# Kernel optimization log

Hardware: AMD Instinct MI355X
Metric: run time of the kernel (lower is better)

The kernel has to match this reference:

```python
import jax, jax.numpy as jnp
import numpy as np

B, K, N = 8192, 10, 100
LAM = 1.0


def _vec_transpose_P():
    # 9x9 vec-transpose permutation: P[3i+j, 3j+i] = 1 (the _getP matrix)
    P = np.zeros((9, 9), dtype=np.float32)
    for i in range(3):
        for j in range(3):
            P[3 * i + j, 3 * j + i] = 1.0
    return jnp.asarray(P)


def setup_inputs() -> dict:
    key = jax.random.key(0)
    k1, k2, k3 = jax.random.split(key, 3)
    weights = jax.random.uniform(k1, (N, 1), dtype=jnp.float32) + 0.1  # positive weights
    model_keypoints = jax.random.normal(k2, (K, 3, N), dtype=jnp.float32)
    y = jax.random.normal(k3, (B, 3, N), dtype=jnp.float32)
    return {"y": y, "weights": weights, "model_keypoints": model_keypoints}


def _pace_forward(y, weights, model_keypoints):
    n = model_keypoints.shape[-1]
    k = model_keypoints.shape[0]
    bsz = y.shape[0]
    w = weights                                  # (N,1)
    wsum = w.sum()
    b = model_keypoints                          # (K,3,N)
    b_w = (b @ w) / wsum                         # (K,3,1)
    sw = jnp.sqrt(w[:, 0])                       # (N,)

    # ---- precomputed constants (original __init__) ----
    bar_b = sw[None, None, :] * (b - b_w)                    # (K,3,N)
    bar_B = bar_b.transpose(0, 2, 1).reshape(k, 3 * n).T     # (3N,K), row idx 3n+a
    bar_H = 2.0 * (bar_B.T @ bar_B + LAM * jnp.eye(k, dtype=y.dtype))
    Hinv = jnp.linalg.inv(bar_H)
    Ht = Hinv @ jnp.ones((k, 1), dtype=y.dtype)
    denom = Ht.sum()
    G = Hinv - (Ht @ Ht.T) / denom               # (K,K)
    g = Ht / denom                               # (K,1)
    GBt = G @ bar_B.T                            # (K,3N)
    M = jnp.concatenate([2.0 * bar_B @ GBt - jnp.eye(3 * n, dtype=y.dtype),
                         2.0 * jnp.sqrt(LAM) * GBt], axis=0)       # (3N+K,3N)
    h = jnp.concatenate([bar_B @ g, jnp.sqrt(LAM) * g], axis=0)    # (3N+K,1)
    P = _vec_transpose_P().astype(y.dtype)

    # ---- forward ----
    y_w = (y @ w) / wsum                         # (B,3,1)
    bar_y = sw[None, None, :] * (y - y_w)        # (B,3,N)

    # E_b = M @ kron(Ybar_b^T, I3) @ P, done batched without materializing kron:
    # (M @ kron(Y^T, I3))[m, 3j+a] = sum_n M[m, 3n+a] * Y[j, n]
    Mr = M.reshape(-1, n, 3)                                  # Mr[m, nn, a] = M[m, 3nn+a]
    MB = jnp.einsum('mna,bjn->bmja', Mr, bar_y)               # (B,3N+K,3,3)
    E = MB.reshape(bsz, -1, 9) @ P                            # (B,3N+K,9)
    q00 = h[:, 0] @ h[:, 0]                                   # scalar h^T h
    hE = jnp.einsum('m,bmc->bc', h[:, 0], E)                  # (B,9)
    Q11 = jnp.einsum('bmc,bmd->bcd', E, E)                    # (B,9,9)
    top = jnp.concatenate([jnp.broadcast_to(q00, (bsz, 1, 1)), hE[:, None, :]], axis=2)
    bot = jnp.concatenate([hE[:, :, None], Q11], axis=2)
    Q = jnp.concatenate([top, bot], axis=1)                   # (B,10,10)

    # SDP relaxation: at a tight optimum X = v v^T with v the minimizer of v^T Q v,
    # recovered here as the eigenvector of Q with smallest eigenvalue (batched eigh)
    _, evec = jnp.linalg.eigh(Q)
    v = evec[:, :, 0]                                         # (B,10), ascending order
    v = v / v[:, :1]                                          # homogenize: v[0] = 1
    R = v[:, 1:].reshape(bsz, 3, 3).transpose(0, 2, 1)        # (B,3,3)

    # shape coefficients: c = 2 * G B^T * kron(I_N, R^T) vec(bar_y) + g
    RTy = jnp.einsum('bra,brn->bna', R, bar_y).reshape(bsz, 3 * n)   # idx 3n+a
    c = 2.0 * jnp.einsum('km,bm->bk', GBt, RTy)[:, :, None] + g[None, :, :]  # (B,K,1)
    # translation: t = y_w - R b_w^T c
    t = y_w - R @ jnp.einsum('ka,bko->bao', b_w[:, :, 0], c)  # (B,3,1)
    return R, t, c


def reference(y, weights, model_keypoints):
    return _pace_forward(y, weights, model_keypoints)
```

## Files before the change

### kernel.cpp

```cpp
#include <hip/hip_runtime.h>
#include <math.h>

#define SM_WSUM 0
#define SM_RWS  1
#define SM_Q00  2
#define SM_Z2   4
#define SM_BS   16
#define SM_W    48
#define SM_G    148
#define SM_GV   248
#define SM_BW   260
#define SM_SIZE 292

__host__ __device__ constexpr int TRI(int p,int q){ return p*10-(p*(p+1))/2+q; }
__host__ __device__ constexpr int SIDX(int a,int b){ return (a<=b)?TRI(a,b):TRI(b,a); }
__host__ __device__ constexpr int LTRI(int i,int j){ return i*(i+1)/2+j; }

template<int CTRL>
__device__ __forceinline__ float dpp_add(float v){
  int s = __builtin_amdgcn_mov_dpp(__float_as_int(v), CTRL, 0xF, 0xF, true);
  return v + __int_as_float(s);
}
__device__ __forceinline__ float gsum8(float v){
  v = dpp_add<0xB1>(v);
  v = dpp_add<0x4E>(v);
  v = dpp_add<0x141>(v);
  return v;
}

__global__ __launch_bounds__(64,1) void pace_fused(const float* __restrict__ y,
                                                   const float* __restrict__ w,
                                                   const float* __restrict__ mk,
                                                   float* __restrict__ out){
  __shared__ __attribute__((aligned(16))) float sc[3600];
  __shared__ float sm[SM_SIZE];
  __shared__ __attribute__((aligned(16))) float scr[3712];
  const int tid  = threadIdx.x;
  const int sub  = tid & 7;
  const int item = tid >> 3;
  const int gb   = blockIdx.x*8 + item;
  const float* yb = y + gb*300;

  {
    float* s_mb = scr;
    float* s_w  = scr+3000;
    float* s_sw = scr+3104;
    float* s_bw = scr+3208;
    float* s_C  = scr+3240;
    float* s_Hi = scr+3340;
    float* s_G  = scr+3440;
    float* s_T  = scr+3540;
    float* s_gv = scr+3640;
    float* s_Ht = scr+3656;
    float* s_z  = scr+3672;

    for (int i=tid;i<3000;i+=64) s_mb[i]=mk[i];
    for (int i=tid;i<100;i+=64){ float x=w[i]; s_w[i]=x; s_sw[i]=sqrtf(x); }
    __syncthreads();

    float a = s_w[tid] + ((tid<36)? s_w[tid+64] : 0.f);
    #pragma unroll
    for (int m=32;m;m>>=1) a += __shfl_xor(a,m);
    const float wsum = a;
    const float rws = 1.0f/a;

    if (tid<30){
      const float4* p=(const float4*)&s_mb[tid*100];
      const float4* q=(const float4*)&s_w[0];
      float acc=0;
      #pragma unroll 5
      for (int j=0;j<25;j++){ float4 x=p[j], yv=q[j];
        acc=fmaf(x.x,yv.x,acc); acc=fmaf(x.y,yv.y,acc);
        acc=fmaf(x.z,yv.z,acc); acc=fmaf(x.w,yv.w,acc); }
      s_bw[tid]=acc*rws;
    }
    __syncthreads();
    for (int i=tid;i<3000;i+=64){ int r=i/100, n=i-r*100; s_mb[i]=s_sw[n]*(s_mb[i]-s_bw[r]); }
    __syncthreads();
    for (int e=tid;e<100;e+=64){
      int k=e/10, k2=e-10*k;
      const float4* p1=(const float4*)&s_mb[k*300];
      const float4* p2=(const float4*)&s_mb[k2*300];
      float acc=0;
      #pragma unroll 5
      for (int j=0;j<75;j++){ float4 x=p1[j], yv=p2[j];
        acc=fmaf(x.x,yv.x,acc); acc=fmaf(x.y,yv.y,acc);
        acc=fmaf(x.z,yv.z,acc); acc=fmaf(x.w,yv.w,acc); }
      s_C[e]=acc;
    }
    __syncthreads();
    float R[20];
    {
      int row=(tid<10)? tid : 0;
      #pragma unroll
      for (int c=0;c<10;c++) R[c]=2.0f*(s_C[row*10+c]+(c==row?1.0f:0.0f));
      #pragma unroll
      for (int c=0;c<10;c++) R[10+c]=(c==row)?1.0f:0.0f;
    }
    #pragma unroll
    for (int p=0;p<10;p++){
      float appv=__shfl(R[p],p);
      float ra=1.0f/appv;
      float fr=R[p];
      #pragma unroll
      for (int c=0;c<20;c++){
        float pc=__shfl(R[c],p)*ra;
        R[c]=(tid==p)? pc : fmaf(-fr,pc,R[c]);
      }
    }
    float ht=0.f;
    if (tid<10){
      #pragma unroll
      for (int c=0;c<10;c++){ s_Hi[tid*10+c]=R[10+c]; ht+=R[10+c]; }
      s_Ht[tid]=ht;
    }
    float hv=(tid<10)? ht : 0.f;
    #pragma unroll
    for (int m=32;m;m>>=1) hv+=__shfl_xor(hv,m);
    const float rden=1.0f/hv;
    if (tid<10) s_gv[tid]=ht*rden;
    __syncthreads();
    for (int e=tid;e<100;e+=64){ int r=e/10,c=e-10*r; s_G[e]=s_Hi[e]-s_Ht[r]*s_Ht[c]*rden; }
    __syncthreads();
    for (int e=tid;e<100;e+=64){
      int r=e/10,c=e-10*r; float acc=0;
      #pragma unroll
      for (int j=0;j<10;j++) acc+=(s_C[r*10+j]+(r==j?1.0f:0.0f))*s_G[j*10+c];
      s_T[e]=acc;
    }
    __syncthreads();
    for (int e=tid;e<100;e+=64){
      int r=e/10,c=e-10*r; float acc=0;
      #pragma unroll
      for (int j=0;j<10;j++) acc+=s_G[r*10+j]*s_T[j*10+c];
      sm[SM_W+e]=4.0f*acc-4.0f*s_G[e];
      sm[SM_G+e]=s_G[e];
    }
    if (tid<10){
      float acc=0;
      #pragma unroll
      for (int j=0;j<10;j++) acc+=(s_C[tid*10+j]+(tid==j?1.0f:0.0f))*s_gv[j];
      s_z[tid]=acc;
    }
    __syncthreads();
    if (tid<10){
      float acc=0;
      #pragma unroll
      for (int j=0;j<10;j++) acc+=s_G[tid*10+j]*s_z[j];
      sm[SM_Z2+tid]=2.0f*acc-s_gv[tid];
    }
    float qv=0.f;
    if (tid<10){
      float acc=0;
      #pragma unroll
      for (int c=0;c<10;c++) acc+=s_C[tid*10+c]*s_gv[c];
      qv=s_gv[tid]*acc+s_gv[tid]*s_gv[tid];
    }
    #pragma unroll
    for (int m=32;m;m>>=1) qv+=__shfl_xor(qv,m);
    if (tid==0){ sm[SM_WSUM]=wsum; sm[SM_RWS]=rws; sm[SM_Q00]=qv; sm[3]=0.f; }
    for (int i=tid;i<3600;i+=64){
      int n=i/36, e=i-36*n; float v;
      if (e==0) v=s_w[n];
      else if (e>=31) v=0.f;
      else v=s_mb[(e-1)*100+n]*s_sw[n];
      sc[i]=v;
    }
    if (tid<30){
      const float4* p=(const float4*)&s_mb[tid*100];
      const float4* q=(const float4*)&s_sw[0];
      float acc=0;
      #pragma unroll 5
      for (int j=0;j<25;j++){ float4 x=p[j], yv=q[j];
        acc=fmaf(x.x,yv.x,acc); acc=fmaf(x.y,yv.y,acc);
        acc=fmaf(x.z,yv.z,acc); acc=fmaf(x.w,yv.w,acc); }
      sm[SM_BS+tid]=acc;
    }
    if (tid<10) sm[SM_GV+tid]=s_gv[tid];
    if (tid<30) sm[SM_BW+tid]=s_bw[tid];
    __syncthreads();
  }

  float* sF  = scr;
  float* sD  = scr+736;
  float* sQl = scr+832;
  float* sG3 = scr+1280;

  float F0[90];
  #pragma unroll
  for (int i=0;i<90;i++) F0[i]=0.f;
  float swy0=0,swy1=0,swy2=0,s00=0,s01=0,s02=0,s11=0,s12=0,s22=0;

  #pragma unroll
  for (int mrep=0;mrep<4;++mrep){
    int g=sub+8*mrep;
    if (g<25){
      float4 a4=*(const float4*)(yb+4*g);
      float4 b4=*(const float4*)(yb+100+4*g);
      float4 g4=*(const float4*)(yb+200+4*g);
      float ax[4]={a4.x,a4.y,a4.z,a4.w};
      float bx[4]={b4.x,b4.y,b4.z,b4.w};
      float gx[4]={g4.x,g4.y,g4.z,g4.w};
      #pragma unroll
      for (int u=0;u<4;u++){
        const float* cf=&sc[(4*g+u)*36];
        float c[32];
        #pragma unroll
        for (int r=0;r<8;r++) ((float4*)c)[r]=((const float4*)cf)[r];
        float y0=ax[u],y1=bx[u],y2=gx[u];
        float wn=c[0];
        float wy0=wn*y0,wy1=wn*y1,wy2=wn*y2;
        swy0+=wy0;swy1+=wy1;swy2+=wy2;
        s00+=wy0*y0;s01+=wy0*y1;s02+=wy0*y2;s11+=wy1*y1;s12+=wy1*y2;s22+=wy2*y2;
        #pragma unroll
        for (int k=0;k<10;k++){
          #pragma unroll
          for (int j=0;j<3;j++){
            float bcv=c[1+k*3+j];
            F0[k*9+j*3+0]+=bcv*y0;
            F0[k*9+j*3+1]+=bcv*y1;
            F0[k*9+j*3+2]+=bcv*y2;
          }
        }
      }
    }
  }
  #pragma unroll
  for (int e=0;e<90;e++) F0[e]=gsum8(F0[e]);
  swy0=gsum8(swy0); swy1=gsum8(swy1); swy2=gsum8(swy2);
  s00=gsum8(s00); s01=gsum8(s01); s02=gsum8(s02);
  s11=gsum8(s11); s12=gsum8(s12); s22=gsum8(s22);

  const float wsum=sm[SM_WSUM], rws=sm[SM_RWS];
  const float yw0=swy0*rws, yw1=swy1*rws, yw2=swy2*rws;
  float G3r[9];
  G3r[0]=s00-wsum*yw0*yw0; G3r[4]=s11-wsum*yw1*yw1; G3r[8]=s22-wsum*yw2*yw2;
  G3r[1]=G3r[3]=s01-wsum*yw0*yw1;
  G3r[2]=G3r[6]=s02-wsum*yw0*yw2;
  G3r[5]=G3r[7]=s12-wsum*yw1*yw2;
  #pragma unroll
  for (int k=0;k<10;k++){
    float bs0=sm[SM_BS+k*3+0],bs1=sm[SM_BS+k*3+1],bs2=sm[SM_BS+k*3+2];
    F0[k*9+0]-=yw0*bs0; F0[k*9+1]-=yw1*bs0; F0[k*9+2]-=yw2*bs0;
    F0[k*9+3]-=yw0*bs1; F0[k*9+4]-=yw1*bs1; F0[k*9+5]-=yw2*bs1;
    F0[k*9+6]-=yw0*bs2; F0[k*9+7]-=yw1*bs2; F0[k*9+8]-=yw2*bs2;
  }
  if (sub==0){
    #pragma unroll
    for (int e=0;e<90;e++) sF[item*90+e]=F0[e];
    #pragma unroll
    for (int e=0;e<9;e++) sG3[item*9+e]=G3r[e];
  }
  __syncthreads();

  {
    int mp=sub;
    float fcol[10], t2[10];
    #pragma unroll
    for (int k=0;k<10;k++) fcol[k]=sF[item*90+k*9+mp];
    #pragma unroll
    for (int k=0;k<10;k++){
      float acc=0;
      #pragma unroll
      for (int k2=0;k2<10;k2++) acc+=sm[SM_W+k*10+k2]*fcol[k2];
      t2[k]=acc;
    }
    float he=0;
    #pragma unroll
    for (int k=0;k<10;k++) he+=sm[SM_Z2+k]*fcol[k];
    sQl[item*56 + 1+mp]=he;
    #pragma unroll 1
    for (int m=0;m<=mp;m++){
      float gd=sG3[item*9+(m%3)*3+(mp%3)];
      float acc=((m/3)==(mp/3))? gd : 0.f;
      #pragma unroll
      for (int k=0;k<10;k++) acc+=sF[item*90+k*9+m]*t2[k];
      int p=1+m, q=1+mp;
      sQl[item*56 + p*10-((p*(p+1))>>1)+q]=acc;
    }
    if (sub==0){
      mp=8;
      #pragma unroll
      for (int k=0;k<10;k++) fcol[k]=sF[item*90+k*9+mp];
      #pragma unroll
      for (int k=0;k<10;k++){
        float acc=0;
        #pragma unroll
        for (int k2=0;k2<10;k2++) acc+=sm[SM_W+k*10+k2]*fcol[k2];
        t2[k]=acc;
      }
      he=0;
      #pragma unroll
      for (int k=0;k<10;k++) he+=sm[SM_Z2+k]*fcol[k];
      sQl[item*56 + 9]=he;
      #pragma unroll 1
      for (int m=0;m<=8;m++){
        float gd=sG3[item*9+(m%3)*3+2];
        float acc=((m/3)==2)? gd : 0.f;
        #pragma unroll
        for (int k=0;k<10;k++) acc+=sF[item*90+k*9+m]*t2[k];
        int p=1+m, q=9;
        sQl[item*56 + p*10-((p*(p+1))>>1)+q]=acc;
      }
      sQl[item*56 + 0]=sm[SM_Q00];
    }
  }
  __syncthreads();

  float A[55];
  #pragma unroll
  for (int e=0;e<55;e++) A[e]=sQl[item*56+e];
  float dd[10], ee[9];
  #pragma unroll
  for (int k=0;k<8;k++){
    float nrm2=0.f;
    #pragma unroll
    for (int i=1;i<10;i++){ if (i<k+1) continue; float xi=A[SIDX(i,k)]; nrm2=fmaf(xi,xi,nrm2); }
    float x0=A[SIDX(k+1,k)];
    float nr=sqrtf(nrm2);
    float alpha=-copysignf(nr,x0);
    bool ok=nrm2>1e-30f;
    float v1=x0-alpha;
    float vtv=-2.0f*alpha*v1;
    float bh=ok?2.0f*__builtin_amdgcn_rcpf(vtv):0.f;
    ee[k]=ok?alpha:x0;
    float vv[10];
    #pragma unroll
    for (int i=0;i<10;i++) vv[i]=(i<k+1)?0.f:((i==k+1)?v1:A[SIDX(i,k)]);
    float p[10];
    #pragma unroll
    for (int i=0;i<10;i++){
      if (i<k+1){ p[i]=0.f; continue; }
      float acc=0;
      #pragma unroll
      for (int j=1;j<10;j++){ if (j<k+1) continue; acc+=A[SIDX(i,j)]*vv[j]; }
      p[i]=bh*acc;
    }
    float Kc=0.f;
    #pragma unroll
    for (int i=1;i<10;i++){ if (i<k+1) continue; Kc=fmaf(vv[i],p[i],Kc); }
    Kc*=0.5f*bh;
    float wv[10];
    #pragma unroll
    for (int i=0;i<10;i++) wv[i]=p[i]-Kc*vv[i];
    #pragma unroll
    for (int i=1;i<10;i++){
      if (i<k+1) continue;
      #pragma unroll
      for (int j=1;j<10;j++){
        if (j<i) continue;
        A[TRI(i,j)]-=vv[i]*wv[j]+wv[i]*vv[j];
      }
    }
  }
  ee[8]=A[TRI(8,9)];
  #pragma unroll
  for (int i=0;i<10;i++) dd[i]=A[TRI(i,i)];
  float esq[9];
  #pragma unroll
  for (int i=0;i<9;i++) esq[i]=ee[i]*ee[i];

  float scaleT=0.f, lo=1e30f, hi=1e30f;
  #pragma unroll
  for (int i=0;i<10;i++){
    float r=((i>0)?fabsf(ee[i-1]):0.f)+((i<9)?fabsf(ee[i]):0.f);
    scaleT=fmaxf(scaleT,fabsf(dd[i])+r);
    lo=fminf(lo,dd[i]-r);
    hi=fminf(hi,dd[i]);
  }
  hi+=1e-6f*scaleT+1e-30f;
  const float pm=1e-12f*scaleT+1e-37f;
  const float r9=1.0f/9.0f;
  #pragma unroll 1
  for (int it=0;it<6;++it){
    float delta=(hi-lo)*r9;
    float mid=lo+delta*(float)(sub+1);
    float q=dd[0]-mid;
    q=(fabsf(q)<pm)?((q<0.f)?-pm:pm):q;
    int cnt=(q<0.f);
    #pragma unroll
    for (int i=1;i<10;i++){
      q=dd[i]-mid-esq[i-1]*__builtin_amdgcn_rcpf(q);
      q=(fabsf(q)<pm)?((q<0.f)?-pm:pm):q;
      cnt+=(q<0.f);
    }
    unsigned long long bal=__ballot(cnt>0);
    unsigned gb8=(unsigned)((bal>>(item*8))&0xFFull);
    int js=gb8?(__ffs((int)gb8)-1):8;
    float nhi=(js<8)?(lo+delta*(float)(js+1)):hi;
    lo=lo+delta*(float)js;
    hi=nhi;
  }
  const float sigma=lo-1e-5f*scaleT-1e-30f;
  const float pmL=1e-8f*scaleT+1e-37f;

  float Lc[55], rd[10];
  #pragma unroll
  for (int i=0;i<10;i++){
    #pragma unroll
    for (int j=0;j<10;j++){
      if (j>i) continue;
      float a=sQl[item*56+SIDX(j,i)]-((i==j)?sigma:0.f);
      #pragma unroll
      for (int t2=0;t2<9;t2++){
        if (t2>=j) continue;
        a-=Lc[LTRI(i,t2)]*Lc[LTRI(j,t2)];
      }
      if (j<i) Lc[LTRI(i,j)]=a*rd[j];
      else { a=fmaxf(a,pmL); rd[i]=rsqrtf(a); Lc[LTRI(i,i)]=a*rd[i]; }
    }
  }
  float xv[10];
  #pragma unroll
  for (int i=0;i<10;i++) xv[i]=1.f;
  #pragma unroll 1
  for (int itr=0;itr<3;++itr){
    #pragma unroll
    for (int i=0;i<10;i++){
      float acc=xv[i];
      #pragma unroll
      for (int j=0;j<9;j++){ if (j>=i) continue; acc-=Lc[LTRI(i,j)]*xv[j]; }
      acc*=rd[i];
      xv[i]=fminf(fmaxf(acc,-1e15f),1e15f);
    }
    #pragma unroll
    for (int i=9;i>=0;i--){
      float acc=xv[i];
      #pragma unroll
      for (int j=9;j>0;j--){ if (j<=i) continue; acc-=Lc[LTRI(j,i)]*xv[j]; }
      acc*=rd[i];
      xv[i]=fminf(fmaxf(acc,-1e15f),1e15f);
    }
    float nn=0.f;
    #pragma unroll
    for (int i=0;i<10;i++) nn=fmaf(xv[i],xv[i],nn);
    nn=fmaxf(nn,1e-30f);
    float sc2=rsqrtf(nn);
    #pragma unroll
    for (int i=0;i<10;i++) xv[i]*=sc2;
  }
  float r0=1.0f/xv[0];
  float vn[10];
  vn[0]=1.f;
  #pragma unroll
  for (int m=1;m<10;m++) vn[m]=xv[m]*r0;

  {
    float dv=0;
    #pragma unroll
    for (int m=0;m<9;m++) dv+=vn[1+m]*sF[item*90+sub*9+m];
    sD[item*10+sub]=dv;
    if (sub<2){
      float dv2=0;
      #pragma unroll
      for (int m=0;m<9;m++) dv2+=vn[1+m]*sF[item*90+(8+sub)*9+m];
      sD[item*10+8+sub]=dv2;
    }
  }
  __syncthreads();
  float dreg[10];
  #pragma unroll
  for (int k=0;k<10;k++) dreg[k]=sD[item*10+k];
  __syncthreads();
  {
    float acc=0;
    #pragma unroll
    for (int k2=0;k2<10;k2++) acc+=sm[SM_G+sub*10+k2]*dreg[k2];
    float cvk=2.0f*acc+sm[SM_GV+sub];
    out[98304+gb*10+sub]=cvk;
    sD[item*10+sub]=cvk;
    if (sub<2){
      int kk=8+sub;
      float acc2=0;
      #pragma unroll
      for (int k2=0;k2<10;k2++) acc2+=sm[SM_G+kk*10+k2]*dreg[k2];
      float cvk2=2.0f*acc2+sm[SM_GV+kk];
      out[98304+gb*10+kk]=cvk2;
      sD[item*10+kk]=cvk2;
    }
  }
  __syncthreads();
  float cvr[10];
  #pragma unroll
  for (int k=0;k<10;k++) cvr[k]=sD[item*10+k];
  float e0=0,e1=0,e2=0;
  #pragma unroll
  for (int k=0;k<10;k++){
    e0+=sm[SM_BW+k*3+0]*cvr[k];
    e1+=sm[SM_BW+k*3+1]*cvr[k];
    e2+=sm[SM_BW+k*3+2]*cvr[k];
  }
  if (sub==2){
    #pragma unroll
    for (int i=0;i<3;i++)
      #pragma unroll
      for (int j=0;j<3;j++)
        out[gb*9+i*3+j]=vn[1+3*j+i];
  }
  if (sub==3){
    out[73728+gb*3+0]=yw0-(vn[1]*e0+vn[4]*e1+vn[7]*e2);
    out[73728+gb*3+1]=yw1-(vn[2]*e0+vn[5]*e1+vn[8]*e2);
    out[73728+gb*3+2]=yw2-(vn[3]*e0+vn[6]*e1+vn[9]*e2);
  }
}

extern "C" void kernel_launch(void* const* d_in, const int* in_sizes, int n_in,
                              void* d_out, int out_size, void* d_ws, size_t ws_size,
                              hipStream_t stream) {
  const float* y  = (const float*)d_in[0];
  const float* w  = (const float*)d_in[1];
  const float* mk = (const float*)d_in[2];
  float* out = (float*)d_out;
  pace_fused<<<1024, 64, 0, stream>>>(y, w, mk, out);
}
```

Baseline: 104.6 us.

## Use 16 lanes per batch item, shrink shared scratch, double grid

Each batch item now gets 16 lanes instead of 8, so a 64-thread block handles 4 items and the grid doubles to 2048 blocks. The per-point accumulation, reductions (gsum16), Q-row construction, bisection (17 intervals, 5 iterations) and final outputs are remapped to the wider group. The preamble no longer stages the full model-keypoint array in LDS: it computes C directly from global memory and writes the weighted coefficients straight into sc, which shrinks shared scratch to allow 2 blocks per CU. The trade-off is that every block now repeats the per-block constant preprocessing, twice as many blocks run it, and more global reads are made in the preamble.

```diff
diff --git a/kernel.cpp b/kernel.cpp
--- a/kernel.cpp
+++ b/kernel.cpp
@@ -12,6 +12,21 @@
 #define SM_BW   260
 #define SM_SIZE 292
 
+#define AR_W    0
+#define AR_BW   104
+#define AR_C    136
+#define AR_HI   240
+#define AR_G    340
+#define AR_T    440
+#define AR_GV   544
+#define AR_HT   560
+#define AR_Z    576
+#define AR_F    0
+#define AR_QL   360
+#define AR_D    592
+#define AR_G3   640
+#define AR_SIZE 768
+
 __host__ __device__ constexpr int TRI(int p,int q){ return p*10-(p*(p+1))/2+q; }
 __host__ __device__ constexpr int SIDX(int a,int b){ return (a<=b)?TRI(a,b):TRI(b,a); }
 __host__ __device__ constexpr int LTRI(int i,int j){ return i*(i+1)/2+j; }
@@ -21,79 +36,95 @@
   int s = __builtin_amdgcn_mov_dpp(__float_as_int(v), CTRL, 0xF, 0xF, true);
   return v + __int_as_float(s);
 }
-__device__ __forceinline__ float gsum8(float v){
+__device__ __forceinline__ float gsum16(float v){
   v = dpp_add<0xB1>(v);
   v = dpp_add<0x4E>(v);
   v = dpp_add<0x141>(v);
+  v = dpp_add<0x140>(v);
   return v;
 }
 
-__global__ __launch_bounds__(64,1) void pace_fused(const float* __restrict__ y,
+__global__ __launch_bounds__(64,2) void pace_fused(const float* __restrict__ y,
                                                    const float* __restrict__ w,
                                                    const float* __restrict__ mk,
                                                    float* __restrict__ out){
   __shared__ __attribute__((aligned(16))) float sc[3600];
   __shared__ float sm[SM_SIZE];
-  __shared__ __attribute__((aligned(16))) float scr[3712];
+  __shared__ __attribute__((aligned(16))) float arena[AR_SIZE];
   const int tid  = threadIdx.x;
-  const int sub  = tid & 7;
-  const int item = tid >> 3;
-  const int gb   = blockIdx.x*8 + item;
+  const int sub  = tid & 15;
+  const int item = tid >> 4;
+  const int gb   = blockIdx.x*4 + item;
   const float* yb = y + gb*300;
 
   {
-    float* s_mb = scr;
-    float* s_w  = scr+3000;
-    float* s_sw = scr+3104;
-    float* s_bw = scr+3208;
-    float* s_C  = scr+3240;
-    float* s_Hi = scr+3340;
-    float* s_G  = scr+3440;
-    float* s_T  = scr+3540;
-    float* s_gv = scr+3640;
-    float* s_Ht = scr+3656;
-    float* s_z  = scr+3672;
-
-    for (int i=tid;i<3000;i+=64) s_mb[i]=mk[i];
-    for (int i=tid;i<100;i+=64){ float x=w[i]; s_w[i]=x; s_sw[i]=sqrtf(x); }
-    __syncthreads();
-
-    float a = s_w[tid] + ((tid<36)? s_w[tid+64] : 0.f);
-    #pragma unroll
-    for (int m=32;m;m>>=1) a += __shfl_xor(a,m);
-    const float wsum = a;
-    const float rws = 1.0f/a;
+    float* a_w  = arena+AR_W;
+    float* a_bw = arena+AR_BW;
+    float* a_C  = arena+AR_C;
+    float* a_Hi = arena+AR_HI;
+    float* a_G  = arena+AR_G;
+    float* a_T  = arena+AR_T;
+    float* a_gv = arena+AR_GV;
+    float* a_Ht = arena+AR_HT;
+    float* a_z  = arena+AR_Z;
+
+    for (int i=tid;i<100;i+=64) a_w[i]=w[i];
+    __syncthreads();
+
+    float av = a_w[tid] + ((tid<36)? a_w[tid+64] : 0.f);
+    #pragma unroll
+    for (int m=32;m;m>>=1) av += __shfl_xor(av,m);
+    const float wsum = av;
+    const float rws  = 1.0f/av;
 
     if (tid<30){
-      const float4* p=(const float4*)&s_mb[tid*100];
-      const float4* q=(const float4*)&s_w[0];
+      const float4* p=(const float4*)(mk+tid*100);
+      const float4* q=(const float4*)a_w;
       float acc=0;
       #pragma unroll 5
       for (int j=0;j<25;j++){ float4 x=p[j], yv=q[j];
         acc=fmaf(x.x,yv.x,acc); acc=fmaf(x.y,yv.y,acc);
         acc=fmaf(x.z,yv.z,acc); acc=fmaf(x.w,yv.w,acc); }
-      s_bw[tid]=acc*rws;
-    }
-    __syncthreads();
-    for (int i=tid;i<3000;i+=64){ int r=i/100, n=i-r*100; s_mb[i]=s_sw[n]*(s_mb[i]-s_bw[r]); }
-    __syncthreads();
+      a_bw[tid]=acc*rws;
+    }
+    __syncthreads();
+
+    for (int i=tid;i<3000;i+=64){
+      int r=i/100, n=i-100*r;
+      sc[n*36+1+r]=a_w[n]*(mk[i]-a_bw[r]);
+    }
+    for (int i=tid;i<100;i+=64){
+      sc[i*36]=a_w[i];
+      sc[i*36+31]=0.f; sc[i*36+32]=0.f; sc[i*36+33]=0.f;
+      sc[i*36+34]=0.f; sc[i*36+35]=0.f;
+    }
     for (int e=tid;e<100;e+=64){
       int k=e/10, k2=e-10*k;
-      const float4* p1=(const float4*)&s_mb[k*300];
-      const float4* p2=(const float4*)&s_mb[k2*300];
-      float acc=0;
-      #pragma unroll 5
-      for (int j=0;j<75;j++){ float4 x=p1[j], yv=p2[j];
-        acc=fmaf(x.x,yv.x,acc); acc=fmaf(x.y,yv.y,acc);
-        acc=fmaf(x.z,yv.z,acc); acc=fmaf(x.w,yv.w,acc); }
-      s_C[e]=acc;
-    }
-    __syncthreads();
+      float acc=0;
+      #pragma unroll
+      for (int j=0;j<3;j++){
+        const float4* pa=(const float4*)(mk+(3*k+j)*100);
+        const float4* pb=(const float4*)(mk+(3*k2+j)*100);
+        const float4* pw=(const float4*)a_w;
+        float ba=a_bw[3*k+j], bb=a_bw[3*k2+j];
+        #pragma unroll 5
+        for (int q=0;q<25;q++){
+          float4 xa=pa[q], xb=pb[q], xw=pw[q];
+          acc=fmaf(xw.x*(xa.x-ba),(xb.x-bb),acc);
+          acc=fmaf(xw.y*(xa.y-ba),(xb.y-bb),acc);
+          acc=fmaf(xw.z*(xa.z-ba),(xb.z-bb),acc);
+          acc=fmaf(xw.w*(xa.w-ba),(xb.w-bb),acc);
+        }
+      }
+      a_C[e]=acc;
+    }
+    __syncthreads();
+
     float R[20];
     {
       int row=(tid<10)? tid : 0;
       #pragma unroll
-      for (int c=0;c<10;c++) R[c]=2.0f*(s_C[row*10+c]+(c==row?1.0f:0.0f));
+      for (int c=0;c<10;c++) R[c]=2.0f*(a_C[row*10+c]+(c==row?1.0f:0.0f));
       #pragma unroll
       for (int c=0;c<10;c++) R[10+c]=(c==row)?1.0f:0.0f;
     }
@@ -111,125 +142,104 @@
     float ht=0.f;
     if (tid<10){
       #pragma unroll
-      for (int c=0;c<10;c++){ s_Hi[tid*10+c]=R[10+c]; ht+=R[10+c]; }
-      s_Ht[tid]=ht;
+      for (int c=0;c<10;c++){ a_Hi[tid*10+c]=R[10+c]; ht+=R[10+c]; }
+      a_Ht[tid]=ht;
     }
     float hv=(tid<10)? ht : 0.f;
     #pragma unroll
     for (int m=32;m;m>>=1) hv+=__shfl_xor(hv,m);
     const float rden=1.0f/hv;
-    if (tid<10) s_gv[tid]=ht*rden;
-    __syncthreads();
-    for (int e=tid;e<100;e+=64){ int r=e/10,c=e-10*r; s_G[e]=s_Hi[e]-s_Ht[r]*s_Ht[c]*rden; }
+    if (tid<10) a_gv[tid]=ht*rden;
+    __syncthreads();
+    for (int e=tid;e<100;e+=64){ int r=e/10,c=e-10*r; a_G[e]=a_Hi[e]-a_Ht[r]*a_Ht[c]*rden; }
     __syncthreads();
     for (int e=tid;e<100;e+=64){
       int r=e/10,c=e-10*r; float acc=0;
       #pragma unroll
-      for (int j=0;j<10;j++) acc+=(s_C[r*10+j]+(r==j?1.0f:0.0f))*s_G[j*10+c];
-      s_T[e]=acc;
+      for (int j=0;j<10;j++) acc+=(a_C[r*10+j]+(r==j?1.0f:0.0f))*a_G[j*10+c];
+      a_T[e]=acc;
     }
     __syncthreads();
     for (int e=tid;e<100;e+=64){
       int r=e/10,c=e-10*r; float acc=0;
       #pragma unroll
-      for (int j=0;j<10;j++) acc+=s_G[r*10+j]*s_T[j*10+c];
-      sm[SM_W+e]=4.0f*acc-4.0f*s_G[e];
-      sm[SM_G+e]=s_G[e];
+      for (int j=0;j<10;j++) acc+=a_G[r*10+j]*a_T[j*10+c];
+      sm[SM_W+e]=4.0f*acc-4.0f*a_G[e];
+      sm[SM_G+e]=a_G[e];
     }
     if (tid<10){
       float acc=0;
       #pragma unroll
-      for (int j=0;j<10;j++) acc+=(s_C[tid*10+j]+(tid==j?1.0f:0.0f))*s_gv[j];
-      s_z[tid]=acc;
+      for (int j=0;j<10;j++) acc+=(a_C[tid*10+j]+(tid==j?1.0f:0.0f))*a_gv[j];
+      a_z[tid]=acc;
     }
     __syncthreads();
     if (tid<10){
       float acc=0;
       #pragma unroll
-      for (int j=0;j<10;j++) acc+=s_G[tid*10+j]*s_z[j];
-      sm[SM_Z2+tid]=2.0f*acc-s_gv[tid];
+      for (int j=0;j<10;j++) acc+=a_G[tid*10+j]*a_z[j];
+      sm[SM_Z2+tid]=2.0f*acc-a_gv[tid];
     }
     float qv=0.f;
     if (tid<10){
       float acc=0;
       #pragma unroll
-      for (int c=0;c<10;c++) acc+=s_C[tid*10+c]*s_gv[c];
-      qv=s_gv[tid]*acc+s_gv[tid]*s_gv[tid];
+      for (int c=0;c<10;c++) acc+=a_C[tid*10+c]*a_gv[c];
+      qv=a_gv[tid]*acc+a_gv[tid]*a_gv[tid];
     }
     #pragma unroll
     for (int m=32;m;m>>=1) qv+=__shfl_xor(qv,m);
     if (tid==0){ sm[SM_WSUM]=wsum; sm[SM_RWS]=rws; sm[SM_Q00]=qv; sm[3]=0.f; }
-    for (int i=tid;i<3600;i+=64){
-      int n=i/36, e=i-36*n; float v;
-      if (e==0) v=s_w[n];
-      else if (e>=31) v=0.f;
-      else v=s_mb[(e-1)*100+n]*s_sw[n];
-      sc[i]=v;
-    }
     if (tid<30){
-      const float4* p=(const float4*)&s_mb[tid*100];
-      const float4* q=(const float4*)&s_sw[0];
-      float acc=0;
-      #pragma unroll 5
-      for (int j=0;j<25;j++){ float4 x=p[j], yv=q[j];
-        acc=fmaf(x.x,yv.x,acc); acc=fmaf(x.y,yv.y,acc);
-        acc=fmaf(x.z,yv.z,acc); acc=fmaf(x.w,yv.w,acc); }
+      float acc=0;
+      for (int n=0;n<100;n++) acc+=sc[n*36+1+tid];
       sm[SM_BS+tid]=acc;
     }
-    if (tid<10) sm[SM_GV+tid]=s_gv[tid];
-    if (tid<30) sm[SM_BW+tid]=s_bw[tid];
-    __syncthreads();
-  }
-
-  float* sF  = scr;
-  float* sD  = scr+736;
-  float* sQl = scr+832;
-  float* sG3 = scr+1280;
+    if (tid<10) sm[SM_GV+tid]=a_gv[tid];
+    if (tid<30) sm[SM_BW+tid]=a_bw[tid];
+    __syncthreads();
+  }
+
+  float* sF  = arena+AR_F;
+  float* sQl = arena+AR_QL;
+  float* sD  = arena+AR_D;
+  float* sG3 = arena+AR_G3;
 
   float F0[90];
   #pragma unroll
   for (int i=0;i<90;i++) F0[i]=0.f;
   float swy0=0,swy1=0,swy2=0,s00=0,s01=0,s02=0,s11=0,s12=0,s22=0;
 
-  #pragma unroll
-  for (int mrep=0;mrep<4;++mrep){
-    int g=sub+8*mrep;
-    if (g<25){
-      float4 a4=*(const float4*)(yb+4*g);
-      float4 b4=*(const float4*)(yb+100+4*g);
-      float4 g4=*(const float4*)(yb+200+4*g);
-      float ax[4]={a4.x,a4.y,a4.z,a4.w};
-      float bx[4]={b4.x,b4.y,b4.z,b4.w};
-      float gx[4]={g4.x,g4.y,g4.z,g4.w};
-      #pragma unroll
-      for (int u=0;u<4;u++){
-        const float* cf=&sc[(4*g+u)*36];
-        float c[32];
-        #pragma unroll
-        for (int r=0;r<8;r++) ((float4*)c)[r]=((const float4*)cf)[r];
-        float y0=ax[u],y1=bx[u],y2=gx[u];
-        float wn=c[0];
-        float wy0=wn*y0,wy1=wn*y1,wy2=wn*y2;
-        swy0+=wy0;swy1+=wy1;swy2+=wy2;
-        s00+=wy0*y0;s01+=wy0*y1;s02+=wy0*y2;s11+=wy1*y1;s12+=wy1*y2;s22+=wy2*y2;
-        #pragma unroll
-        for (int k=0;k<10;k++){
-          #pragma unroll
-          for (int j=0;j<3;j++){
-            float bcv=c[1+k*3+j];
-            F0[k*9+j*3+0]+=bcv*y0;
-            F0[k*9+j*3+1]+=bcv*y1;
-            F0[k*9+j*3+2]+=bcv*y2;
-          }
-        }
+  auto point=[&](int n){
+    float y0=yb[n], y1=yb[100+n], y2=yb[200+n];
+    float c[32];
+    const float4* cp=(const float4*)&sc[n*36];
+    #pragma unroll
+    for (int r=0;r<8;r++) ((float4*)c)[r]=cp[r];
+    float wn=c[0];
+    float wy0=wn*y0,wy1=wn*y1,wy2=wn*y2;
+    swy0+=wy0;swy1+=wy1;swy2+=wy2;
+    s00+=wy0*y0;s01+=wy0*y1;s02+=wy0*y2;s11+=wy1*y1;s12+=wy1*y2;s22+=wy2*y2;
+    #pragma unroll
+    for (int k=0;k<10;k++){
+      #pragma unroll
+      for (int j=0;j<3;j++){
+        float bcv=c[1+k*3+j];
+        F0[k*9+j*3+0]+=bcv*y0;
+        F0[k*9+j*3+1]+=bcv*y1;
+        F0[k*9+j*3+2]+=bcv*y2;
       }
     }
-  }
-  #pragma unroll
-  for (int e=0;e<90;e++) F0[e]=gsum8(F0[e]);
-  swy0=gsum8(swy0); swy1=gsum8(swy1); swy2=gsum8(swy2);
-  s00=gsum8(s00); s01=gsum8(s01); s02=gsum8(s02);
-  s11=gsum8(s11); s12=gsum8(s12); s22=gsum8(s22);
+  };
+  #pragma unroll
+  for (int m=0;m<6;m++) point(sub+16*m);
+  if (sub<4) point(96+sub);
+
+  #pragma unroll
+  for (int e=0;e<90;e++) F0[e]=gsum16(F0[e]);
+  swy0=gsum16(swy0); swy1=gsum16(swy1); swy2=gsum16(swy2);
+  s00=gsum16(s00); s01=gsum16(s01); s02=gsum16(s02);
+  s11=gsum16(s11); s12=gsum16(s12); s22=gsum16(s22);
 
   const float wsum=sm[SM_WSUM], rws=sm[SM_RWS];
   const float yw0=swy0*rws, yw1=swy1*rws, yw2=swy2*rws;
@@ -253,7 +263,7 @@
   }
   __syncthreads();
 
-  {
+  if (sub<9){
     int mp=sub;
     float fcol[10], t2[10];
     #pragma unroll
@@ -278,33 +288,8 @@
       int p=1+m, q=1+mp;
       sQl[item*56 + p*10-((p*(p+1))>>1)+q]=acc;
     }
-    if (sub==0){
-      mp=8;
-      #pragma unroll
-      for (int k=0;k<10;k++) fcol[k]=sF[item*90+k*9+mp];
-      #pragma unroll
-      for (int k=0;k<10;k++){
-        float acc=0;
-        #pragma unroll
-        for (int k2=0;k2<10;k2++) acc+=sm[SM_W+k*10+k2]*fcol[k2];
-        t2[k]=acc;
-      }
-      he=0;
-      #pragma unroll
-      for (int k=0;k<10;k++) he+=sm[SM_Z2+k]*fcol[k];
-      sQl[item*56 + 9]=he;
-      #pragma unroll 1
-      for (int m=0;m<=8;m++){
-        float gd=sG3[item*9+(m%3)*3+2];
-        float acc=((m/3)==2)? gd : 0.f;
-        #pragma unroll
-        for (int k=0;k<10;k++) acc+=sF[item*90+k*9+m]*t2[k];
-        int p=1+m, q=9;
-        sQl[item*56 + p*10-((p*(p+1))>>1)+q]=acc;
-      }
-      sQl[item*56 + 0]=sm[SM_Q00];
-    }
-  }
+  }
+  if (sub==9) sQl[item*56 + 0]=sm[SM_Q00];
   __syncthreads();
 
   float A[55];
@@ -370,10 +355,10 @@
   }
   hi+=1e-6f*scaleT+1e-30f;
   const float pm=1e-12f*scaleT+1e-37f;
-  const float r9=1.0f/9.0f;
+  const float r17=1.0f/17.0f;
   #pragma unroll 1
-  for (int it=0;it<6;++it){
-    float delta=(hi-lo)*r9;
+  for (int it=0;it<5;++it){
+    float delta=(hi-lo)*r17;
     float mid=lo+delta*(float)(sub+1);
     float q=dd[0]-mid;
     q=(fabsf(q)<pm)?((q<0.f)?-pm:pm):q;
@@ -385,9 +370,9 @@
       cnt+=(q<0.f);
     }
     unsigned long long bal=__ballot(cnt>0);
-    unsigned gb8=(unsigned)((bal>>(item*8))&0xFFull);
-    int js=gb8?(__ffs((int)gb8)-1):8;
-    float nhi=(js<8)?(lo+delta*(float)(js+1)):hi;
+    unsigned gm=(unsigned)((bal>>(item*16))&0xFFFFull);
+    int js=gm?(__ffs((int)gm)-1):16;
+    float nhi=(js<16)?(lo+delta*(float)(js+1)):hi;
     lo=lo+delta*(float)js;
     hi=nhi;
   }
@@ -445,44 +430,29 @@
   #pragma unroll
   for (int m=1;m<10;m++) vn[m]=xv[m]*r0;
 
-  {
+  if (sub<10){
     float dv=0;
     #pragma unroll
     for (int m=0;m<9;m++) dv+=vn[1+m]*sF[item*90+sub*9+m];
-    sD[item*10+sub]=dv;
-    if (sub<2){
-      float dv2=0;
-      #pragma unroll
-      for (int m=0;m<9;m++) dv2+=vn[1+m]*sF[item*90+(8+sub)*9+m];
-      sD[item*10+8+sub]=dv2;
-    }
+    sD[item*12+sub]=dv;
   }
   __syncthreads();
   float dreg[10];
   #pragma unroll
-  for (int k=0;k<10;k++) dreg[k]=sD[item*10+k];
+  for (int k=0;k<10;k++) dreg[k]=sD[item*12+k];
   __syncthreads();
-  {
+  if (sub<10){
     float acc=0;
     #pragma unroll
     for (int k2=0;k2<10;k2++) acc+=sm[SM_G+sub*10+k2]*dreg[k2];
     float cvk=2.0f*acc+sm[SM_GV+sub];
     out[98304+gb*10+sub]=cvk;
-    sD[item*10+sub]=cvk;
-    if (sub<2){
-      int kk=8+sub;
-      float acc2=0;
-      #pragma unroll
-      for (int k2=0;k2<10;k2++) acc2+=sm[SM_G+kk*10+k2]*dreg[k2];
-      float cvk2=2.0f*acc2+sm[SM_GV+kk];
-      out[98304+gb*10+kk]=cvk2;
-      sD[item*10+kk]=cvk2;
-    }
+    sD[item*12+sub]=cvk;
   }
   __syncthreads();
   float cvr[10];
   #pragma unroll
-  for (int k=0;k<10;k++) cvr[k]=sD[item*10+k];
+  for (int k=0;k<10;k++) cvr[k]=sD[item*12+k];
   float e0=0,e1=0,e2=0;
   #pragma unroll
   for (int k=0;k<10;k++){
@@ -490,14 +460,14 @@
     e1+=sm[SM_BW+k*3+1]*cvr[k];
     e2+=sm[SM_BW+k*3+2]*cvr[k];
   }
-  if (sub==2){
+  if (sub==10){
     #pragma unroll
     for (int i=0;i<3;i++)
       #pragma unroll
       for (int j=0;j<3;j++)
         out[gb*9+i*3+j]=vn[1+3*j+i];
   }
-  if (sub==3){
+  if (sub==11){
     out[73728+gb*3+0]=yw0-(vn[1]*e0+vn[4]*e1+vn[7]*e2);
     out[73728+gb*3+1]=yw1-(vn[2]*e0+vn[5]*e1+vn[8]*e2);
     out[73728+gb*3+2]=yw2-(vn[3]*e0+vn[6]*e1+vn[9]*e2);
@@ -511,5 +481,5 @@
   const float* w  = (const float*)d_in[1];
   const float* mk = (const float*)d_in[2];
   float* out = (float*)d_out;
-  pace_fused<<<1024, 64, 0, stream>>>(y, w, mk, out);
+  pace_fused<<<2048, 64, 0, stream>>>(y, w, mk, out);
 }
```

After: 110.1 us. 5.3% more time.
